# Optimization experiments

Measured on AMD Instinct MI355X. Metric: run time of the kernel, lower is better.

The kernel has to match this reference:

```python
import jax, jax.numpy as jnp
import numpy as np

ALPHA = 1.0   # inherent_params['alpha']
H_COUP = 0.1  # inherent_params['h']
DT = 0.01     # inherent_params['dt']
N = 4096      # inherent_params['n_oscillators']


def setup_inputs() -> dict:
    key = jax.random.key(0)
    ks = jax.random.split(key, 10)
    n = N
    x_old = 0.01 * jax.random.normal(ks[0], (n, 1), dtype=jnp.float32)
    y_old = 0.01 * jax.random.normal(ks[1], (n, 1), dtype=jnp.float32)
    x_old_dot = jax.random.normal(ks[2], (n, 1), dtype=jnp.float32)
    omega = 0.5 + 2.0 * jax.random.uniform(ks[3], (n, 1), dtype=jnp.float32)
    A = 0.5 + jax.random.uniform(ks[4], (n, 1), dtype=jnp.float32)
    b = 0.1 * jax.random.normal(ks[5], (n, 1), dtype=jnp.float32)
    h_a = 0.2 * jax.random.uniform(ks[6], (n, 1), dtype=jnp.float32)
    phase_diffs = jnp.pi * jax.random.normal(ks[7], (n, n), dtype=jnp.float32)
    x_state = 0.01 * jax.random.normal(ks[8], (n, 1), dtype=jnp.float32)
    y_state = 0.01 * jax.random.normal(ks[9], (n, 1), dtype=jnp.float32)
    return {"x_old": x_old, "y_old": y_old, "x_old_dot": x_old_dot,
            "omega": omega, "A": A, "b": b, "h_a": h_a,
            "phase_diffs": phase_diffs, "x_state": x_state, "y_state": y_state}


def reference(x_old, y_old, x_old_dot, omega, A, b, h_a, phase_diffs, x_state, y_state):
    n = x_old.shape[0]
    idx = jnp.arange(n)
    # init-time: zero the phase-diff diagonal
    pd = phase_diffs.at[idx, idx].set(0.0)

    r_sq = x_old ** 2 + (y_old - b) ** 2                       # [n,1]
    zeta = 1.0 - h_a * (x_old / (jnp.abs(x_old_dot) + 1e-9))   # [n,1]
    k_diag = ALPHA * (1.0 - r_sq)                              # [n,1]

    kd = k_diag[:, 0]
    wz = omega[:, 0] / zeta[:, 0]
    # block-diagonal K: 2x2 blocks [[kd, -wz], [wz, kd]]
    K = jnp.zeros((2 * n, 2 * n), dtype=x_old.dtype)
    K = K.at[2 * idx, 2 * idx].set(kd).at[2 * idx + 1, 2 * idx + 1].set(kd)
    K = K.at[2 * idx, 2 * idx + 1].set(-wz).at[2 * idx + 1, 2 * idx].set(wz)

    # coupling R: h * rotation(phase_diffs[i,j]) in each 2x2 block
    c, s = jnp.cos(pd), jnp.sin(pd)                            # [n,n]
    blocks = jnp.stack([jnp.stack([c, -s], axis=-1),
                        jnp.stack([s, c], axis=-1)], axis=-2)  # [n,n,2,2]
    R = H_COUP * blocks.transpose(0, 2, 1, 3).reshape(2 * n, 2 * n)

    # state vector: torch cat(dim=1).T.reshape(-1,1) -> [x_all; (y-b)_all] block order
    sv = jnp.concatenate([x_old[:, 0], (y_old - b)[:, 0]])[:, None]  # [2n,1]
    dot = (K + R) @ sv                                          # [2n,1] matvec

    # constraint: clamp by 2*omega, interleaved (repeat_interleave)
    max_full = jnp.repeat(2.0 * omega[:, 0], 2)[:, None]        # [2n,1]
    dot = jnp.clip(dot, -max_full, max_full)

    y_new = y_state + (dot[1::2] + b) * DT                      # [n,1]
    return A * y_new
```

## Files before the change

### kernel.cpp

```cpp
#include <hip/hip_runtime.h>
#include <math.h>

#define NN 4096
#define ALPHA_C 1.0f
#define H_COUP_C 0.1f
#define DT_C 0.01f
#define RPB 4

__global__ __launch_bounds__(256) void cpg_fused(
        const float* __restrict__ pd,
        const float* __restrict__ x_old,
        const float* __restrict__ y_old,
        const float* __restrict__ x_old_dot,
        const float* __restrict__ omega,
        const float* __restrict__ A,
        const float* __restrict__ b,
        const float* __restrict__ h_a,
        const float* __restrict__ y_state,
        float* __restrict__ out) {
    const int tid = threadIdx.x;

    __shared__ float lds_uv[2 * NN];
    __shared__ float wsum[4][RPB];

    const float4* x4 = reinterpret_cast<const float4*>(x_old);
    const float4* y4 = reinterpret_cast<const float4*>(y_old);
    const float4* b4 = reinterpret_cast<const float4*>(b);
    #pragma unroll
    for (int k = 0; k < 8; ++k) {
        int m = k * 256 + tid;
        float4 t4;
        if (m < 1024) {
            t4 = x4[m];
        } else {
            float4 ya = y4[m - 1024];
            float4 bb = b4[m - 1024];
            t4 = make_float4(ya.x - bb.x, ya.y - bb.y, ya.z - bb.z, ya.w - bb.w);
        }
        int s0 = (m >> 1) + (m & 1) * 2048;
        int s1 = s0 + 1024;
        *reinterpret_cast<float2*>(&lds_uv[2 * s0]) = make_float2(t4.x, t4.y);
        *reinterpret_cast<float2*>(&lds_uv[2 * s1]) = make_float2(t4.z, t4.w);
    }
    __syncthreads();

    const int row0 = blockIdx.x * RPB;
    const float* __restrict__ prow = pd + (size_t)row0 * NN;
    float acc[RPB] = {0.f, 0.f, 0.f, 0.f};
    #pragma unroll
    for (int k = 0; k < 4; ++k) {
        const int sbase = k * 256 + tid;
        const int jb = sbase * 4;
        float2 uv0 = *reinterpret_cast<const float2*>(&lds_uv[2 * sbase]);
        float2 uv1 = *reinterpret_cast<const float2*>(&lds_uv[2 * (sbase + 1024)]);
        float2 uv2 = *reinterpret_cast<const float2*>(&lds_uv[2 * (sbase + 2048)]);
        float2 uv3 = *reinterpret_cast<const float2*>(&lds_uv[2 * (sbase + 3072)]);
        #pragma unroll
        for (int r = 0; r < RPB; ++r) {
            float4 p4 = *reinterpret_cast<const float4*>(prow + (size_t)r * NN + jb);
            float a = acc[r];
            a = fmaf(__sinf(p4.x), uv0.x, a);
            a = fmaf(__cosf(p4.x), uv0.y, a);
            a = fmaf(__sinf(p4.y), uv1.x, a);
            a = fmaf(__cosf(p4.y), uv1.y, a);
            a = fmaf(__sinf(p4.z), uv2.x, a);
            a = fmaf(__cosf(p4.z), uv2.y, a);
            a = fmaf(__sinf(p4.w), uv3.x, a);
            a = fmaf(__cosf(p4.w), uv3.y, a);
            acc[r] = a;
        }
    }

    #pragma unroll
    for (int r = 0; r < RPB; ++r) {
        #pragma unroll
        for (int off = 32; off > 0; off >>= 1)
            acc[r] += __shfl_xor(acc[r], off, 64);
    }
    const int wid = tid >> 6;
    if ((tid & 63) == 0) {
        #pragma unroll
        for (int r = 0; r < RPB; ++r) wsum[wid][r] = acc[r];
    }
    __syncthreads();

    if (tid < RPB) {
        const int r = tid;
        const int i = row0 + r;
        float total = wsum[0][r] + wsum[1][r] + wsum[2][r] + wsum[3][r];
        int si = (i >> 2) + (i & 3) * 1024;
        float2 uvi = *reinterpret_cast<const float2*>(&lds_uv[2 * si]);
        float pii = pd[(size_t)i * NN + i];
        total -= __sinf(pii) * uvi.x + __cosf(pii) * uvi.y;
        total += uvi.y;

        float xo = x_old[i], yo = y_old[i], bi = b[i];
        float ym = yo - bi;
        float r_sq = xo * xo + ym * ym;
        float kd = ALPHA_C * (1.0f - r_sq);
        float zeta = 1.0f - h_a[i] * (xo / (fabsf(x_old_dot[i]) + 1e-9f));
        float wz = omega[i] / zeta;
        float dot = kd * uvi.y + wz * uvi.x + H_COUP_C * total;
        float m = 2.0f * omega[i];
        dot = fminf(fmaxf(dot, -m), m);
        float y_new = y_state[i] + (dot + bi) * DT_C;
        out[i] = A[i] * y_new;
    }
}

extern "C" void kernel_launch(void* const* d_in, const int* in_sizes, int n_in,
                              void* d_out, int out_size, void* d_ws, size_t ws_size,
                              hipStream_t stream) {
    const float* x_old     = (const float*)d_in[0];
    const float* y_old     = (const float*)d_in[1];
    const float* x_old_dot = (const float*)d_in[2];
    const float* omega     = (const float*)d_in[3];
    const float* A         = (const float*)d_in[4];
    const float* b         = (const float*)d_in[5];
    const float* h_a       = (const float*)d_in[6];
    const float* pd        = (const float*)d_in[7];
    const float* y_state   = (const float*)d_in[9];
    float* out = (float*)d_out;

    cpg_fused<<<NN / RPB, 256, 0, stream>>>(pd, x_old, y_old, x_old_dot,
                                            omega, A, b, h_a, y_state, out);
}
```

Measured before the change: 17.77 us.

## Prefetch phase-diff rows with nontemporal loads and double buffering, double rows per block

Issues the first chunk of phase-diff loads before the LDS staging of the state vector, so the global loads overlap that staging. Each later chunk is prefetched into a second register buffer while the current one is processed. The loads are marked nontemporal and rows per block go from 4 to 8, which halves the grid to 512 blocks. Register pressure rises with 2x8 float4 buffers, so occupancy may drop, and fewer blocks may underfill the CUs.

```diff
diff --git a/kernel.cpp b/kernel.cpp
--- a/kernel.cpp
+++ b/kernel.cpp
@@ -5,7 +5,9 @@
 #define ALPHA_C 1.0f
 #define H_COUP_C 0.1f
 #define DT_C 0.01f
-#define RPB 4
+#define RPB 8
+
+typedef float floatx4 __attribute__((ext_vector_type(4)));
 
 __global__ __launch_bounds__(256) void cpg_fused(
         const float* __restrict__ pd,
@@ -19,62 +21,86 @@
         const float* __restrict__ y_state,
         float* __restrict__ out) {
     const int tid = threadIdx.x;
+    const int row0 = blockIdx.x * RPB;
+    const float* __restrict__ prow = pd + (size_t)row0 * NN;
 
     __shared__ float lds_uv[2 * NN];
     __shared__ float wsum[4][RPB];
 
-    const float4* x4 = reinterpret_cast<const float4*>(x_old);
-    const float4* y4 = reinterpret_cast<const float4*>(y_old);
-    const float4* b4 = reinterpret_cast<const float4*>(b);
+    #define NTLD4(p) __builtin_nontemporal_load(reinterpret_cast<const floatx4*>(p))
+
+    floatx4 cur[RPB];
     #pragma unroll
-    for (int k = 0; k < 8; ++k) {
-        int m = k * 256 + tid;
-        float4 t4;
-        if (m < 1024) {
-            t4 = x4[m];
-        } else {
-            float4 ya = y4[m - 1024];
-            float4 bb = b4[m - 1024];
-            t4 = make_float4(ya.x - bb.x, ya.y - bb.y, ya.z - bb.z, ya.w - bb.w);
+    for (int r = 0; r < RPB; ++r)
+        cur[r] = NTLD4(prow + (size_t)r * NN + tid * 4);
+
+    {
+        const float4* x4 = reinterpret_cast<const float4*>(x_old);
+        const float4* y4 = reinterpret_cast<const float4*>(y_old);
+        const float4* b4 = reinterpret_cast<const float4*>(b);
+        #pragma unroll
+        for (int k = 0; k < 8; ++k) {
+            int m = k * 256 + tid;
+            float4 t4;
+            if (m < 1024) {
+                t4 = x4[m];
+            } else {
+                float4 ya = y4[m - 1024];
+                float4 bb = b4[m - 1024];
+                t4 = make_float4(ya.x - bb.x, ya.y - bb.y, ya.z - bb.z, ya.w - bb.w);
+            }
+            int s0 = (m >> 1) + (m & 1) * 2048;
+            int s1 = s0 + 1024;
+            *reinterpret_cast<float2*>(&lds_uv[2 * s0]) = make_float2(t4.x, t4.y);
+            *reinterpret_cast<float2*>(&lds_uv[2 * s1]) = make_float2(t4.z, t4.w);
         }
-        int s0 = (m >> 1) + (m & 1) * 2048;
-        int s1 = s0 + 1024;
-        *reinterpret_cast<float2*>(&lds_uv[2 * s0]) = make_float2(t4.x, t4.y);
-        *reinterpret_cast<float2*>(&lds_uv[2 * s1]) = make_float2(t4.z, t4.w);
     }
     __syncthreads();
 
-    const int row0 = blockIdx.x * RPB;
-    const float* __restrict__ prow = pd + (size_t)row0 * NN;
-    float acc[RPB] = {0.f, 0.f, 0.f, 0.f};
+    float acc[RPB];
+    #pragma unroll
+    for (int r = 0; r < RPB; ++r) acc[r] = 0.f;
+
     #pragma unroll
     for (int k = 0; k < 4; ++k) {
         const int sbase = k * 256 + tid;
-        const int jb = sbase * 4;
+        floatx4 nxt[RPB];
+        if (k < 3) {
+            const int jn = (k + 1) * 1024 + tid * 4;
+            #pragma unroll
+            for (int r = 0; r < RPB; ++r)
+                nxt[r] = NTLD4(prow + (size_t)r * NN + jn);
+        }
         float2 uv0 = *reinterpret_cast<const float2*>(&lds_uv[2 * sbase]);
         float2 uv1 = *reinterpret_cast<const float2*>(&lds_uv[2 * (sbase + 1024)]);
         float2 uv2 = *reinterpret_cast<const float2*>(&lds_uv[2 * (sbase + 2048)]);
         float2 uv3 = *reinterpret_cast<const float2*>(&lds_uv[2 * (sbase + 3072)]);
+
         #pragma unroll
         for (int r = 0; r < RPB; ++r) {
-            float4 p4 = *reinterpret_cast<const float4*>(prow + (size_t)r * NN + jb);
             float a = acc[r];
-            a = fmaf(__sinf(p4.x), uv0.x, a);
-            a = fmaf(__cosf(p4.x), uv0.y, a);
-            a = fmaf(__sinf(p4.y), uv1.x, a);
-            a = fmaf(__cosf(p4.y), uv1.y, a);
-            a = fmaf(__sinf(p4.z), uv2.x, a);
-            a = fmaf(__cosf(p4.z), uv2.y, a);
-            a = fmaf(__sinf(p4.w), uv3.x, a);
-            a = fmaf(__cosf(p4.w), uv3.y, a);
+            a = fmaf(__sinf(cur[r].x), uv0.x, a);
+            a = fmaf(__cosf(cur[r].x), uv0.y, a);
+            a = fmaf(__sinf(cur[r].y), uv1.x, a);
+            a = fmaf(__cosf(cur[r].y), uv1.y, a);
+            a = fmaf(__sinf(cur[r].z), uv2.x, a);
+            a = fmaf(__cosf(cur[r].z), uv2.y, a);
+            a = fmaf(__sinf(cur[r].w), uv3.x, a);
+            a = fmaf(__cosf(cur[r].w), uv3.y, a);
             acc[r] = a;
         }
+
+        if (k < 3) {
+            #pragma unroll
+            for (int r = 0; r < RPB; ++r) cur[r] = nxt[r];
+        }
     }
+    #undef NTLD4
 
     #pragma unroll
-    for (int r = 0; r < RPB; ++r) {
+    for (int off = 32; off > 0; off >>= 1) {
         #pragma unroll
-        for (int off = 32; off > 0; off >>= 1)
+        for (int r = 0; r < RPB; ++r)
             acc[r] += __shfl_xor(acc[r], off, 64);
     }
     const int wid = tid >> 6;
```

Result: faster. 15.69 us (median of 2 runs) (-11.7%).
